# Optimization experiments

Measured on AMD Instinct MI355X. Metric: run time of the kernel, lower is better.

## Reference

```python
import jax, jax.numpy as jnp
import numpy as np

NE, NR, NT = 100000, 500, 365
DE = DR = DT = 200
P = min(DE, DR, DT)  # 200
B = 1024


def setup_inputs() -> dict:
    key = jax.random.key(0)
    ks = jax.random.split(key, 10)
    return {
        "e1_idx": jax.random.randint(ks[0], (B,), 0, NE),
        "r_idx": jax.random.randint(ks[1], (B,), 0, NR),
        "t_idx": jax.random.randint(ks[2], (B,), 0, NT),
        "E": jax.random.normal(ks[3], (NE, DE), dtype=jnp.float32),
        "R": jax.random.normal(ks[4], (NR, DR), dtype=jnp.float32),
        "T": jax.random.normal(ks[5], (NT, DT), dtype=jnp.float32),
        "F0": jax.random.uniform(ks[6], (DR, P), jnp.float32, -0.1, 0.1),
        "F1": jax.random.uniform(ks[7], (DE, P), jnp.float32, -0.1, 0.1),
        "F2": jax.random.uniform(ks[8], (DE, P), jnp.float32, -0.1, 0.1),
        "F3": jax.random.uniform(ks[9], (DT, P), jnp.float32, -0.1, 0.1),
    }


def reference(e1_idx, r_idx, t_idx, E, R, T, F0, F1, F2, F3):
    # Embedding lookups
    e1 = E[e1_idx]          # (B, de)
    r = R[r_idx]            # (B, dr)
    t = T[t_idx]            # (B, dt)
    # Factor projections into rank-P CPD space
    fr = r @ F0             # (B, P)
    fe1 = e1 @ F1           # (B, P)
    ft = t @ F3             # (B, P)
    FE = E @ F2             # (NE, P)
    # Diagonal core tensor I => the mm/bmm chain is exactly an
    # elementwise product over the rank dimension, then score vs all entities.
    x = (fr * fe1 * ft) @ FE.T  # (B, NE)
    return jax.nn.sigmoid(x)
```

## Files before the change

kernel.cpp:

```cpp
#include <hip/hip_runtime.h>

#define NE_  100000
#define NB_  1024
#define DD_  200
#define PP_  224

typedef _Float16 h8  __attribute__((ext_vector_type(8)));
typedef float    fx4 __attribute__((ext_vector_type(4)));
typedef float    fx16 __attribute__((ext_vector_type(16)));

__device__ __forceinline__ float fast_sigmoid(float x) {
    float e = __builtin_amdgcn_exp2f(-1.44269504088896340736f * x);
    return __builtin_amdgcn_rcpf(1.0f + e);
}

__global__ __launch_bounds__(256) void prep_kernel(
    const int*   __restrict__ e1_idx, const int* __restrict__ r_idx,
    const int*   __restrict__ t_idx,
    const float* __restrict__ E, const float* __restrict__ R,
    const float* __restrict__ T,
    const float* __restrict__ F0, const float* __restrict__ F1,
    const float* __restrict__ F2, const float* __restrict__ F3,
    _Float16* __restrict__ g16)
{
    __shared__ __align__(16) float hl[4][DD_];
    const int tid = threadIdx.x;
    const int rb  = blockIdx.x * 4;

    const float* rrow[4];
    const float* erow[4];
    const float* trow[4];
    #pragma unroll
    for (int i = 0; i < 4; ++i) {
        rrow[i] = R + (size_t)r_idx[rb + i]  * DD_;
        erow[i] = E + (size_t)e1_idx[rb + i] * DD_;
        trow[i] = T + (size_t)t_idx[rb + i]  * DD_;
    }

    const int p = tid;
    if (p < DD_) {
        float fr[4], fe[4], ft[4];
        #pragma unroll
        for (int i = 0; i < 4; ++i) { fr[i] = 0.f; fe[i] = 0.f; ft[i] = 0.f; }
        #pragma unroll 4
        for (int k = 0; k < DD_; ++k) {
            float f0 = F0[k * DD_ + p];
            float f1 = F1[k * DD_ + p];
            float f3 = F3[k * DD_ + p];
            #pragma unroll
            for (int i = 0; i < 4; ++i) {
                fr[i] = fmaf(rrow[i][k], f0, fr[i]);
                fe[i] = fmaf(erow[i][k], f1, fe[i]);
                ft[i] = fmaf(trow[i][k], f3, ft[i]);
            }
        }
        #pragma unroll
        for (int i = 0; i < 4; ++i)
            hl[i][p] = fr[i] * fe[i] * ft[i];
    }
    __syncthreads();

    const int j = tid;
    if (j < PP_) {
        float g[4] = {0.f, 0.f, 0.f, 0.f};
        if (j < DD_) {
            const float* f2r = F2 + (size_t)j * DD_;
            for (int p4 = 0; p4 < DD_; p4 += 4) {
                fx4 f2v = *(const fx4*)(f2r + p4);
                #pragma unroll
                for (int i = 0; i < 4; ++i) {
                    fx4 hv = *(const fx4*)&hl[i][p4];
                    g[i] = fmaf(hv[0], f2v[0], g[i]);
                    g[i] = fmaf(hv[1], f2v[1], g[i]);
                    g[i] = fmaf(hv[2], f2v[2], g[i]);
                    g[i] = fmaf(hv[3], f2v[3], g[i]);
                }
            }
        }
        #pragma unroll
        for (int i = 0; i < 4; ++i)
            g16[(size_t)(rb + i) * PP_ + j] = (_Float16)g[i];
    }
}

__global__ __launch_bounds__(256, 4) void score_kernel(
    const _Float16* __restrict__ g16, const float* __restrict__ E,
    float* __restrict__ out)
{
    __shared__ __align__(16) _Float16 Alds[64 * 232];

    const int tid = threadIdx.x;
    const int w   = tid >> 6;
    const int l   = tid & 63;
    const int l31 = l & 31;
    const int lh  = l >> 5;
    const int wm  = w & 1;
    const int wn  = w >> 1;
    const int nb  = blockIdx.x * 64;

    h8 bfr[13];
    {
        int n = nb + wn * 32 + l31;
        if (n >= NE_) n = NE_ - 1;
        const float* ep = E + (size_t)n * DD_;
        #pragma unroll
        for (int ks = 0; ks < 13; ++ks) {
            const int k = ks * 16 + lh * 8;
            h8 v = {(_Float16)0, (_Float16)0, (_Float16)0, (_Float16)0,
                    (_Float16)0, (_Float16)0, (_Float16)0, (_Float16)0};
            if (k < DD_) {
                fx4 lo = *(const fx4*)(ep + k);
                fx4 hi = *(const fx4*)(ep + k + 4);
                v[0] = (_Float16)lo[0]; v[1] = (_Float16)lo[1];
                v[2] = (_Float16)lo[2]; v[3] = (_Float16)lo[3];
                v[4] = (_Float16)hi[0]; v[5] = (_Float16)hi[1];
                v[6] = (_Float16)hi[2]; v[7] = (_Float16)hi[3];
            }
            bfr[ks] = v;
        }
    }

    const int ncol = nb + wn * 32 + l31;
    const bool nok = (ncol < NE_);
    const int srow = tid >> 2;
    const int scol = (tid & 3) * 8;

    for (int c = 0; c < 16; ++c) {
        __syncthreads();
        const _Float16* gsrc = g16 + (size_t)(c * 64) * PP_;
        #pragma unroll
        for (int j = 0; j < 7; ++j)
            *(h8*)&Alds[srow * 232 + scol + j * 32] =
                *(const h8*)(gsrc + (size_t)srow * PP_ + scol + j * 32);
        __syncthreads();

        fx16 acc;
        #pragma unroll
        for (int i = 0; i < 16; ++i) acc[i] = 0.0f;

        #pragma unroll
        for (int ks = 0; ks < 13; ++ks) {
            h8 a = *(const h8*)&Alds[(wm * 32 + l31) * 232 + ks * 16 + lh * 8];
            acc = __builtin_amdgcn_mfma_f32_32x32x16_f16(a, bfr[ks], acc, 0, 0, 0);
        }

        if (nok) {
            const int mb = c * 64 + wm * 32 + lh * 4;
            #pragma unroll
            for (int r = 0; r < 16; ++r) {
                int m = mb + (r & 3) + 8 * (r >> 2);
                out[(size_t)m * NE_ + ncol] = fast_sigmoid(acc[r]);
            }
        }
    }
}

extern "C" void kernel_launch(void* const* d_in, const int* in_sizes, int n_in,
                              void* d_out, int out_size, void* d_ws, size_t ws_size,
                              hipStream_t stream)
{
    const int*   e1_idx = (const int*)  d_in[0];
    const int*   r_idx  = (const int*)  d_in[1];
    const int*   t_idx  = (const int*)  d_in[2];
    const float* E      = (const float*)d_in[3];
    const float* R      = (const float*)d_in[4];
    const float* T      = (const float*)d_in[5];
    const float* F0     = (const float*)d_in[6];
    const float* F1     = (const float*)d_in[7];
    const float* F2     = (const float*)d_in[8];
    const float* F3     = (const float*)d_in[9];
    float* out = (float*)d_out;

    _Float16* g16 = (_Float16*)d_ws;

    prep_kernel<<<256, 256, 0, stream>>>(e1_idx, r_idx, t_idx, E, R, T,
                                         F0, F1, F2, F3, g16);

    const int nblocks = (NE_ + 63) / 64;
    score_kernel<<<nblocks, 256, 0, stream>>>(g16, E, out);
}
```

Measured before the change: 566.4 us.

## Widen score tile to 128 entities per block and prefetch g16 tiles into registers

The score kernel now has each wave own two 32-column entity tiles, so every A fragment read from LDS feeds two MFMAs. The next 64-row tile of g16 is loaded into registers while the current one is being computed, hiding global load latency. The prep kernel handles 8 query rows per block instead of 4, which halves the prep grid. In exchange, register pressure rises (two sets of B fragments and two accumulators), occupancy drops to 2 blocks per CU, and the score grid halves to 782 blocks.

New measurement: 635.8 us. 1.12x slower.

```diff
diff --git a/kernel.cpp b/kernel.cpp
--- a/kernel.cpp
+++ b/kernel.cpp
@@ -23,15 +23,15 @@
     const float* __restrict__ F2, const float* __restrict__ F3,
     _Float16* __restrict__ g16)
 {
-    __shared__ __align__(16) float hl[4][DD_];
+    __shared__ __align__(16) float hl[8][DD_];
     const int tid = threadIdx.x;
-    const int rb  = blockIdx.x * 4;
-
-    const float* rrow[4];
-    const float* erow[4];
-    const float* trow[4];
+    const int rb  = blockIdx.x * 8;
+
+    const float* rrow[8];
+    const float* erow[8];
+    const float* trow[8];
     #pragma unroll
-    for (int i = 0; i < 4; ++i) {
+    for (int i = 0; i < 8; ++i) {
         rrow[i] = R + (size_t)r_idx[rb + i]  * DD_;
         erow[i] = E + (size_t)e1_idx[rb + i] * DD_;
         trow[i] = T + (size_t)t_idx[rb + i]  * DD_;
@@ -39,36 +39,36 @@
 
     const int p = tid;
     if (p < DD_) {
-        float fr[4], fe[4], ft[4];
-        #pragma unroll
-        for (int i = 0; i < 4; ++i) { fr[i] = 0.f; fe[i] = 0.f; ft[i] = 0.f; }
+        float fr[8], fe[8], ft[8];
+        #pragma unroll
+        for (int i = 0; i < 8; ++i) { fr[i] = 0.f; fe[i] = 0.f; ft[i] = 0.f; }
         #pragma unroll 4
         for (int k = 0; k < DD_; ++k) {
             float f0 = F0[k * DD_ + p];
             float f1 = F1[k * DD_ + p];
             float f3 = F3[k * DD_ + p];
             #pragma unroll
-            for (int i = 0; i < 4; ++i) {
+            for (int i = 0; i < 8; ++i) {
                 fr[i] = fmaf(rrow[i][k], f0, fr[i]);
                 fe[i] = fmaf(erow[i][k], f1, fe[i]);
                 ft[i] = fmaf(trow[i][k], f3, ft[i]);
             }
         }
         #pragma unroll
-        for (int i = 0; i < 4; ++i)
+        for (int i = 0; i < 8; ++i)
             hl[i][p] = fr[i] * fe[i] * ft[i];
     }
     __syncthreads();
 
     const int j = tid;
     if (j < PP_) {
-        float g[4] = {0.f, 0.f, 0.f, 0.f};
+        float g[8] = {0.f, 0.f, 0.f, 0.f, 0.f, 0.f, 0.f, 0.f};
         if (j < DD_) {
             const float* f2r = F2 + (size_t)j * DD_;
             for (int p4 = 0; p4 < DD_; p4 += 4) {
                 fx4 f2v = *(const fx4*)(f2r + p4);
                 #pragma unroll
-                for (int i = 0; i < 4; ++i) {
+                for (int i = 0; i < 8; ++i) {
                     fx4 hv = *(const fx4*)&hl[i][p4];
                     g[i] = fmaf(hv[0], f2v[0], g[i]);
                     g[i] = fmaf(hv[1], f2v[1], g[i]);
@@ -78,12 +78,12 @@
             }
         }
         #pragma unroll
-        for (int i = 0; i < 4; ++i)
+        for (int i = 0; i < 8; ++i)
             g16[(size_t)(rb + i) * PP_ + j] = (_Float16)g[i];
     }
 }
 
-__global__ __launch_bounds__(256, 4) void score_kernel(
+__global__ __launch_bounds__(256, 2) void score_kernel(
     const _Float16* __restrict__ g16, const float* __restrict__ E,
     float* __restrict__ out)
 {
@@ -96,61 +96,86 @@
     const int lh  = l >> 5;
     const int wm  = w & 1;
     const int wn  = w >> 1;
-    const int nb  = blockIdx.x * 64;
-
-    h8 bfr[13];
+    const int nb  = blockIdx.x * 128;
+
+    h8 bfr0[13], bfr1[13];
     {
-        int n = nb + wn * 32 + l31;
-        if (n >= NE_) n = NE_ - 1;
-        const float* ep = E + (size_t)n * DD_;
+        int n0 = nb + wn * 64 + l31;
+        int n1 = n0 + 32;
+        if (n0 >= NE_) n0 = NE_ - 1;
+        if (n1 >= NE_) n1 = NE_ - 1;
+        const float* ep0 = E + (size_t)n0 * DD_;
+        const float* ep1 = E + (size_t)n1 * DD_;
         #pragma unroll
         for (int ks = 0; ks < 13; ++ks) {
             const int k = ks * 16 + lh * 8;
-            h8 v = {(_Float16)0, (_Float16)0, (_Float16)0, (_Float16)0,
-                    (_Float16)0, (_Float16)0, (_Float16)0, (_Float16)0};
+            h8 v0 = {(_Float16)0, (_Float16)0, (_Float16)0, (_Float16)0,
+                     (_Float16)0, (_Float16)0, (_Float16)0, (_Float16)0};
+            h8 v1 = v0;
             if (k < DD_) {
-                fx4 lo = *(const fx4*)(ep + k);
-                fx4 hi = *(const fx4*)(ep + k + 4);
-                v[0] = (_Float16)lo[0]; v[1] = (_Float16)lo[1];
-                v[2] = (_Float16)lo[2]; v[3] = (_Float16)lo[3];
-                v[4] = (_Float16)hi[0]; v[5] = (_Float16)hi[1];
-                v[6] = (_Float16)hi[2]; v[7] = (_Float16)hi[3];
+                fx4 lo0 = *(const fx4*)(ep0 + k);
+                fx4 hi0 = *(const fx4*)(ep0 + k + 4);
+                fx4 lo1 = *(const fx4*)(ep1 + k);
+                fx4 hi1 = *(const fx4*)(ep1 + k + 4);
+                v0[0] = (_Float16)lo0[0]; v0[1] = (_Float16)lo0[1];
+                v0[2] = (_Float16)lo0[2]; v0[3] = (_Float16)lo0[3];
+                v0[4] = (_Float16)hi0[0]; v0[5] = (_Float16)hi0[1];
+                v0[6] = (_Float16)hi0[2]; v0[7] = (_Float16)hi0[3];
+                v1[0] = (_Float16)lo1[0]; v1[1] = (_Float16)lo1[1];
+                v1[2] = (_Float16)lo1[2]; v1[3] = (_Float16)lo1[3];
+                v1[4] = (_Float16)hi1[0]; v1[5] = (_Float16)hi1[1];
+                v1[6] = (_Float16)hi1[2]; v1[7] = (_Float16)hi1[3];
             }
-            bfr[ks] = v;
-        }
-    }
-
-    const int ncol = nb + wn * 32 + l31;
-    const bool nok = (ncol < NE_);
+            bfr0[ks] = v0;
+            bfr1[ks] = v1;
+        }
+    }
+
+    const int ncol0 = nb + wn * 64 + l31;
+    const int ncol1 = ncol0 + 32;
+    const bool nok0 = (ncol0 < NE_);
+    const bool nok1 = (ncol1 < NE_);
+
     const int srow = tid >> 2;
     const int scol = (tid & 3) * 8;
+    const _Float16* gsb = g16 + (size_t)srow * PP_ + scol;
+
+    h8 st[7];
+    #pragma unroll
+    for (int j = 0; j < 7; ++j)
+        st[j] = *(const h8*)(gsb + j * 32);
 
     for (int c = 0; c < 16; ++c) {
         __syncthreads();
-        const _Float16* gsrc = g16 + (size_t)(c * 64) * PP_;
         #pragma unroll
         for (int j = 0; j < 7; ++j)
-            *(h8*)&Alds[srow * 232 + scol + j * 32] =
-                *(const h8*)(gsrc + (size_t)srow * PP_ + scol + j * 32);
+            *(h8*)&Alds[srow * 232 + scol + j * 32] = st[j];
         __syncthreads();
 
-        fx16 acc;
-        #pragma unroll
-        for (int i = 0; i < 16; ++i) acc[i] = 0.0f;
+        if (c + 1 < 16) {
+            const _Float16* gn = gsb + (size_t)((c + 1) * 64) * PP_;
+            #pragma unroll
+            for (int j = 0; j < 7; ++j)
+                st[j] = *(const h8*)(gn + j * 32);
+        }
+
+        fx16 acc0, acc1;
+        #pragma unroll
+        for (int i = 0; i < 16; ++i) { acc0[i] = 0.0f; acc1[i] = 0.0f; }
 
         #pragma unroll
         for (int ks = 0; ks < 13; ++ks) {
             h8 a = *(const h8*)&Alds[(wm * 32 + l31) * 232 + ks * 16 + lh * 8];
-            acc = __builtin_amdgcn_mfma_f32_32x32x16_f16(a, bfr[ks], acc, 0, 0, 0);
-        }
-
-        if (nok) {
-            const int mb = c * 64 + wm * 32 + lh * 4;
-            #pragma unroll
-            for (int r = 0; r < 16; ++r) {
-                int m = mb + (r & 3) + 8 * (r >> 2);
-                out[(size_t)m * NE_ + ncol] = fast_sigmoid(acc[r]);
-            }
+            acc0 = __builtin_amdgcn_mfma_f32_32x32x16_f16(a, bfr0[ks], acc0, 0, 0, 0);
+            acc1 = __builtin_amdgcn_mfma_f32_32x32x16_f16(a, bfr1[ks], acc1, 0, 0, 0);
+        }
+
+        const int mb = c * 64 + wm * 32 + lh * 4;
+        #pragma unroll
+        for (int r = 0; r < 16; ++r) {
+            int m = mb + (r & 3) + 8 * (r >> 2);
+            if (nok0) out[(size_t)m * NE_ + ncol0] = fast_sigmoid(acc0[r]);
+            if (nok1) out[(size_t)m * NE_ + ncol1] = fast_sigmoid(acc1[r]);
         }
     }
 }
@@ -173,9 +198,9 @@
 
     _Float16* g16 = (_Float16*)d_ws;
 
-    prep_kernel<<<256, 256, 0, stream>>>(e1_idx, r_idx, t_idx, E, R, T,
+    prep_kernel<<<128, 256, 0, stream>>>(e1_idx, r_idx, t_idx, E, R, T,
                                          F0, F1, F2, F3, g16);
 
-    const int nblocks = (NE_ + 63) / 64;
+    const int nblocks = (NE_ + 127) / 128;
     score_kernel<<<nblocks, 256, 0, stream>>>(g16, E, out);
 }
```
